# Optimization experiments

Hardware: AMD Instinct MI355X
Metric: run time of the kernel (lower is better)

The kernel has to match this reference:

```python
import jax, jax.numpy as jnp
import numpy as np

N_NODES = 100000
N_EDGES = 3200000
IN_DIM, HID_DIM, OUT_DIM = 512, 32, 16


def spmm(rows, cols, vals, dense):
    # out[r] = sum_{e: rows[e]==r} vals[e] * dense[cols[e]]  == adj @ dense (COO)
    gathered = vals[:, None] * dense[cols]          # [E, D]
    return jax.ops.segment_sum(gathered, rows, num_segments=N_NODES)


def gcn_layer(x, adj_rows, adj_cols, adj_vals, W):
    support = x @ W                                  # dense mm [N, out]
    return spmm(adj_rows, adj_cols, adj_vals, support)


def setup_inputs() -> dict:
    key = jax.random.key(0)
    ks = jax.random.split(key, 8)
    x = jax.random.normal(ks[0], (N_NODES, IN_DIM), dtype=jnp.float32)
    adj_rows = jax.random.randint(ks[1], (N_EDGES,), 0, N_NODES, dtype=jnp.int32)
    adj_cols = jax.random.randint(ks[2], (N_EDGES,), 0, N_NODES, dtype=jnp.int32)
    adj_vals = jax.random.uniform(ks[3], (N_EDGES,), dtype=jnp.float32)
    W1 = jax.random.normal(ks[4], (IN_DIM, HID_DIM), dtype=jnp.float32)
    W2 = jax.random.normal(ks[5], (HID_DIM, OUT_DIM), dtype=jnp.float32)
    W3 = jax.random.normal(ks[6], (OUT_DIM, HID_DIM), dtype=jnp.float32)
    W4 = jax.random.normal(ks[7], (HID_DIM, IN_DIM), dtype=jnp.float32)
    return {"x": x, "adj_rows": adj_rows, "adj_cols": adj_cols,
            "adj_vals": adj_vals, "W1": W1, "W2": W2, "W3": W3, "W4": W4}


def reference(x, adj_rows, adj_cols, adj_vals, W1, W2, W3, W4):
    encoded1 = gcn_layer(x, adj_rows, adj_cols, adj_vals, W1)        # [N, 32]
    encoded2 = gcn_layer(encoded1, adj_rows, adj_cols, adj_vals, W2) # [N, 16]
    decoded1 = gcn_layer(encoded2, adj_rows, adj_cols, adj_vals, W3) # [N, 32]
    decoded2 = gcn_layer(decoded1, adj_rows, adj_cols, adj_vals, W4) # [N, 512]
    return (decoded2, encoded2)
```

## Files before the change

### kernel.cpp

```cpp
#include <hip/hip_runtime.h>
#include <hip/hip_bf16.h>


#define N_NODES 100000
#define N_EDGES 3200000
#define RPB_LOG 7
#define RPB (1 << RPB_LOG)
#define NB ((N_NODES + RPB - 1) / RPB)
#define CHUNK 16384
#define NCHUNK ((N_EDGES + CHUNK - 1) / CHUNK)
#define STAGE_CAP 8192

typedef __attribute__((ext_vector_type(4))) float f32x4;
typedef __attribute__((ext_vector_type(8))) short s16x8;
typedef __attribute__((ext_vector_type(8))) unsigned short u16x8;
typedef __attribute__((ext_vector_type(4))) unsigned short u16x4;
typedef __attribute__((ext_vector_type(4))) int i32x4;

static __device__ inline s16x8 cvt8(const float4& lo, const float4& hi) {
  unsigned p0, p1, p2, p3;
  asm("v_cvt_pk_bf16_f32 %0, %1, %2" : "=v"(p0) : "v"(lo.x), "v"(lo.y));
  asm("v_cvt_pk_bf16_f32 %0, %1, %2" : "=v"(p1) : "v"(lo.z), "v"(lo.w));
  asm("v_cvt_pk_bf16_f32 %0, %1, %2" : "=v"(p2) : "v"(hi.x), "v"(hi.y));
  asm("v_cvt_pk_bf16_f32 %0, %1, %2" : "=v"(p3) : "v"(hi.z), "v"(hi.w));
  i32x4 pi = {(int)p0, (int)p1, (int)p2, (int)p3};
  return __builtin_bit_cast(s16x8, pi);
}

static __device__ inline unsigned pk2(float a, float b) {
  unsigned p;
  asm("v_cvt_pk_bf16_f32 %0, %1, %2" : "=v"(p) : "v"(a), "v"(b));
  return p;
}
static __device__ inline float b2f(unsigned short u) {
  return __uint_as_float(((unsigned)u) << 16);
}

__global__ __launch_bounds__(256) void wconv12_kernel(
    const float* __restrict__ W1, const float* __restrict__ W2,
    uint4* __restrict__ Wfrag) {
  int s = blockIdx.x * 256 + threadIdx.x;
  if (s >= 1024) return;
  int lane = s & 63, kt = s >> 6;
  int n = lane & 15;
  int kb = kt * 32 + (lane >> 4) * 8;
  unsigned p[4];
#pragma unroll
  for (int i = 0; i < 4; ++i) {
    float lo = 0.f, hi = 0.f;
#pragma unroll
    for (int m = 0; m < 32; ++m) {
      float w2 = W2[m * 16 + n];
      lo += W1[(kb + 2 * i) * 32 + m] * w2;
      hi += W1[(kb + 2 * i + 1) * 32 + m] * w2;
    }
    p[i] = pk2(lo, hi);
  }
  Wfrag[s] = make_uint4(p[0], p[1], p[2], p[3]);
}

__global__ __launch_bounds__(256) void mm1_kernel(
    const float* __restrict__ x, const uint4* __restrict__ Wfrag,
    unsigned short* __restrict__ out) {
  const int t = threadIdx.x;
  const int lane = t & 63;
  const int w = t >> 6;
  const int rbase = blockIdx.x * 128 + w * 32;
  const int lrow = lane & 15;
  const int kg = lane >> 4;

  int r0c = rbase + lrow;       if (r0c > N_NODES - 1) r0c = N_NODES - 1;
  int r1c = rbase + 16 + lrow;  if (r1c > N_NODES - 1) r1c = N_NODES - 1;
  const float* xp0 = x + (size_t)r0c * 512 + kg * 8;
  const float* xp1 = x + (size_t)r1c * 512 + kg * 8;
  const s16x8* Wf = (const s16x8*)Wfrag;

  f32x4 acc0 = {0.f, 0.f, 0.f, 0.f}, acc1 = {0.f, 0.f, 0.f, 0.f};

#pragma unroll 4
  for (int kt = 0; kt < 16; ++kt) {
    float4 a0lo = *(const float4*)(xp0 + kt * 32);
    float4 a0hi = *(const float4*)(xp0 + kt * 32 + 4);
    float4 a1lo = *(const float4*)(xp1 + kt * 32);
    float4 a1hi = *(const float4*)(xp1 + kt * 32 + 4);
    s16x8 b = Wf[kt * 64 + lane];
    s16x8 a0 = cvt8(a0lo, a0hi);
    s16x8 a1 = cvt8(a1lo, a1hi);
    acc0 = __builtin_amdgcn_mfma_f32_16x16x32_bf16(a0, b, acc0, 0, 0, 0);
    acc1 = __builtin_amdgcn_mfma_f32_16x16x32_bf16(a1, b, acc1, 0, 0, 0);
  }

  const int col = lane & 15;
#pragma unroll
  for (int reg = 0; reg < 4; ++reg) {
    int r0 = rbase + kg * 4 + reg;
    if (r0 < N_NODES)
      out[(size_t)r0 * 16 + col] = (unsigned short)(pk2(acc0[reg], acc0[reg]) & 0xFFFF);
    int r1 = rbase + 16 + kg * 4 + reg;
    if (r1 < N_NODES)
      out[(size_t)r1 * 16 + col] = (unsigned short)(pk2(acc1[reg], acc1[reg]) & 0xFFFF);
  }
}

__global__ __launch_bounds__(512) void localsort_kernel(
    const int* __restrict__ rows, const int* __restrict__ cols,
    const float* __restrict__ vals, int2* __restrict__ cv_loc,
    int* __restrict__ ofs) {
  __shared__ int lcnt[NB];
  __shared__ int lofs[NB + 1];
  __shared__ int ssum[512];
  const int c = blockIdx.x, t = threadIdx.x;
  const int c0 = c * CHUNK, c1 = min(c0 + CHUNK, N_EDGES);

  for (int i = t; i < NB; i += 512) lcnt[i] = 0;
  __syncthreads();
  for (int e = c0 + t; e < c1; e += 512)
    atomicAdd(&lcnt[rows[e] >> RPB_LOG], 1);
  __syncthreads();

  int v0 = (2 * t < NB) ? lcnt[2 * t] : 0;
  int v1 = (2 * t + 1 < NB) ? lcnt[2 * t + 1] : 0;
  ssum[t] = v0 + v1;
  __syncthreads();
  for (int off = 1; off < 512; off <<= 1) {
    int xv = (t >= off) ? ssum[t - off] : 0;
    __syncthreads();
    ssum[t] += xv;
    __syncthreads();
  }
  int excl = (t == 0) ? 0 : ssum[t - 1];
  if (2 * t < NB) lofs[2 * t] = excl;
  if (2 * t + 1 < NB) lofs[2 * t + 1] = excl + v0;
  if (t == 511) lofs[NB] = ssum[511];
  __syncthreads();

  for (int i = t; i <= NB; i += 512) ofs[c * (NB + 1) + i] = lofs[i];
  for (int i = t; i < NB; i += 512) lcnt[i] = 0;
  __syncthreads();

  for (int e = c0 + t; e < c1; e += 512) {
    int r = rows[e];
    int b = r >> RPB_LOG;
    int rank = atomicAdd(&lcnt[b], 1);
    cv_loc[c0 + lofs[b] + rank] =
        make_int2(((r & (RPB - 1)) << 17) | cols[e], __float_as_int(vals[e]));
  }
}

__global__ __launch_bounds__(1024) void totals_scan_kernel(
    const int* __restrict__ ofs, int* __restrict__ bstart,
    int* __restrict__ row_ptr) {
  __shared__ int s[1024];
  int t = threadIdx.x;
  int tot = 0;
  if (t < NB) {
    for (int cc = 0; cc < NCHUNK; ++cc) {
      const int* o = ofs + cc * (NB + 1);
      tot += o[t + 1] - o[t];
    }
  }
  s[t] = tot;
  __syncthreads();
  for (int off = 1; off < 1024; off <<= 1) {
    int v = (t >= off) ? s[t - off] : 0;
    __syncthreads();
    s[t] += v;
    __syncthreads();
  }
  if (t < NB) bstart[t] = s[t] - tot;
  if (t == 0) { bstart[NB] = N_EDGES; row_ptr[N_NODES] = N_EDGES; }
}

__global__ __launch_bounds__(256) void refine2_kernel(
    const int* __restrict__ ofs, const int* __restrict__ bstart,
    const int2* __restrict__ cv_loc, int2* __restrict__ cv_csr,
    int* __restrict__ row_ptr) {
  __shared__ int gs[NCHUNK];
  __shared__ int q[NCHUNK + 1];
  __shared__ int sq[256];
  __shared__ int rcnt[RPB];
  __shared__ int rbase[RPB];
  __shared__ int2 stage[STAGE_CAP];
  const int b = blockIdx.x, t = threadIdx.x;

  int cnt_t = 0;
  if (t < NCHUNK) {
    int g0 = ofs[t * (NB + 1) + b];
    int g1 = ofs[t * (NB + 1) + b + 1];
    gs[t] = t * CHUNK + g0;
    cnt_t = g1 - g0;
  }
  sq[t] = cnt_t;
  __syncthreads();
  for (int off = 1; off < 256; off <<= 1) {
    int v = (t >= off) ? sq[t - off] : 0;
    __syncthreads();
    sq[t] += v;
    __syncthreads();
  }
  if (t < NCHUNK) q[t] = sq[t] - cnt_t;
  if (t == 0) q[NCHUNK] = sq[255];
  if (t < RPB) rcnt[t] = 0;
  __syncthreads();
  const int Q = q[NCHUNK];

  for (int i = t; i < Q; i += 256) {
    int lo = 0, hi = NCHUNK - 1;
    while (lo < hi) {
      int mid = (lo + hi + 1) >> 1;
      if (q[mid] <= i) lo = mid; else hi = mid - 1;
    }
    int2 e = cv_loc[gs[lo] + (i - q[lo])];
    if (i < STAGE_CAP) stage[i] = e;
    atomicAdd(&rcnt[e.x >> 17], 1);
  }
  __syncthreads();

  int rv = (t < RPB) ? rcnt[t] : 0;
  sq[t] = rv;
  __syncthreads();
  for (int off = 1; off < RPB; off <<= 1) {
    int v = (t >= off) ? sq[t - off] : 0;
    __syncthreads();
    sq[t] += v;
    __syncthreads();
  }
  if (t < RPB) {
    int base = bstart[b] + sq[t] - rv;
    rbase[t] = base;
    int gr = (b << RPB_LOG) + t;
    if (gr < N_NODES) row_ptr[gr] = base;
    rcnt[t] = 0;
  }
  __syncthreads();

  for (int i = t; i < Q; i += 256) {
    int2 e;
    if (i < STAGE_CAP) {
      e = stage[i];
    } else {
      int lo = 0, hi = NCHUNK - 1;
      while (lo < hi) {
        int mid = (lo + hi + 1) >> 1;
        if (q[mid] <= i) lo = mid; else hi = mid - 1;
      }
      e = cv_loc[gs[lo] + (i - q[lo])];
    }
    int rl = e.x >> 17;
    int rank = atomicAdd(&rcnt[rl], 1);
    cv_csr[rbase[rl] + rank] = make_int2(e.x & 0x1FFFF, e.y);
  }
}

template <int OM>
__global__ __launch_bounds__(256) void spmm_b16_kernel(
    const int* __restrict__ rp, const int2* __restrict__ colval,
    const unsigned short* __restrict__ in, unsigned short* __restrict__ outb,
    float* __restrict__ outf) {
  const int t = threadIdx.x;
  const int r = blockIdx.x * 64 + (t >> 2);
  const int q = t & 3;
  if (r >= N_NODES) return;
  const int k0 = rp[r], k1 = rp[r + 1];
  float a0 = 0.f, a1 = 0.f, a2 = 0.f, a3 = 0.f;

  int k = k0;
  for (; k + 7 < k1; k += 8) {
    int2 cv[8];
#pragma unroll
    for (int u = 0; u < 8; ++u) cv[u] = colval[k + u];
    u16x4 g[8];
#pragma unroll
    for (int u = 0; u < 8; ++u)
      g[u] = *(const u16x4*)(in + (size_t)cv[u].x * 16 + q * 4);
#pragma unroll
    for (int u = 0; u < 8; ++u) {
      float v = __int_as_float(cv[u].y);
      a0 += v * b2f(g[u][0]);
      a1 += v * b2f(g[u][1]);
      a2 += v * b2f(g[u][2]);
      a3 += v * b2f(g[u][3]);
    }
  }
  for (; k + 1 < k1; k += 2) {
    int2 cva = colval[k], cvb = colval[k + 1];
    u16x4 ga = *(const u16x4*)(in + (size_t)cva.x * 16 + q * 4);
    u16x4 gb = *(const u16x4*)(in + (size_t)cvb.x * 16 + q * 4);
    float va = __int_as_float(cva.y), vb = __int_as_float(cvb.y);
    a0 += va * b2f(ga[0]); a1 += va * b2f(ga[1]);
    a2 += va * b2f(ga[2]); a3 += va * b2f(ga[3]);
    a0 += vb * b2f(gb[0]); a1 += vb * b2f(gb[1]);
    a2 += vb * b2f(gb[2]); a3 += vb * b2f(gb[3]);
  }
  if (k < k1) {
    int2 cv = colval[k];
    u16x4 g = *(const u16x4*)(in + (size_t)cv.x * 16 + q * 4);
    float v = __int_as_float(cv.y);
    a0 += v * b2f(g[0]); a1 += v * b2f(g[1]);
    a2 += v * b2f(g[2]); a3 += v * b2f(g[3]);
  }

  if (OM == 0 || OM == 1) {
    uint2 pk = make_uint2(pk2(a0, a1), pk2(a2, a3));
    *(uint2*)(outb + (size_t)r * 16 + q * 4) = pk;
  }
  if (OM == 1 || OM == 2) {
    *(float4*)(outf + (size_t)r * 16 + q * 4) = make_float4(a0, a1, a2, a3);
  }
}

__global__ __launch_bounds__(512) void mm4_kernel(
    const float* __restrict__ t3, const float* __restrict__ W3,
    const float* __restrict__ W4, float* __restrict__ out,
    int rows_per_block) {
  const int j = threadIdx.x;
  float w4c[32];
#pragma unroll
  for (int m = 0; m < 32; ++m) w4c[m] = W4[m * 512 + j];
  float w[16];
#pragma unroll
  for (int k = 0; k < 16; ++k) {
    float acc = 0.f;
#pragma unroll
    for (int m = 0; m < 32; ++m) acc += W3[k * 32 + m] * w4c[m];
    w[k] = acc;
  }
  int r0 = blockIdx.x * rows_per_block;
  int r1 = r0 + rows_per_block;
  if (r1 > N_NODES) r1 = N_NODES;
  for (int r = r0; r < r1; ++r) {
    const float* srow = t3 + (size_t)r * 16;
    float a0 = 0.f, a1 = 0.f, a2 = 0.f, a3 = 0.f;
#pragma unroll
    for (int k = 0; k < 16; k += 4) {
      a0 += srow[k + 0] * w[k + 0];
      a1 += srow[k + 1] * w[k + 1];
      a2 += srow[k + 2] * w[k + 2];
      a3 += srow[k + 3] * w[k + 3];
    }
    out[(size_t)r * 512 + j] = (a0 + a1) + (a2 + a3);
  }
}

extern "C" void kernel_launch(void* const* d_in, const int* in_sizes, int n_in,
                              void* d_out, int out_size, void* d_ws, size_t ws_size,
                              hipStream_t stream) {
  const float* x     = (const float*)d_in[0];
  const int*   arows = (const int*)d_in[1];
  const int*   acols = (const int*)d_in[2];
  const float* avals = (const float*)d_in[3];
  const float* W1    = (const float*)d_in[4];
  const float* W2    = (const float*)d_in[5];
  const float* W3    = (const float*)d_in[6];
  const float* W4    = (const float*)d_in[7];

  float* out = (float*)d_out;
  float* dec = out;
  float* enc = out + (size_t)N_NODES * 512;

  unsigned short* bh  = (unsigned short*)d_ws;
  unsigned short* bu  = bh + (size_t)N_NODES * 16;
  unsigned short* be  = bu + (size_t)N_NODES * 16;
  unsigned short* bt2 = be + (size_t)N_NODES * 16;
  float*          t3  = (float*)(bt2 + (size_t)N_NODES * 16);

  int2*  cv_loc  = (int2*)dec;
  int2*  cv_csr  = cv_loc + N_EDGES;
  uint4* Wfrag   = (uint4*)(cv_csr + N_EDGES);
  int*   ofs     = (int*)(Wfrag + 1024);
  int*   row_ptr = ofs + NCHUNK * (NB + 1);
  int*   bstart  = row_ptr + N_NODES + 1;

  wconv12_kernel<<<4, 256, 0, stream>>>(W1, W2, Wfrag);
  localsort_kernel<<<NCHUNK, 512, 0, stream>>>(arows, acols, avals, cv_loc, ofs);
  totals_scan_kernel<<<1, 1024, 0, stream>>>(ofs, bstart, row_ptr);
  refine2_kernel<<<NB, 256, 0, stream>>>(ofs, bstart, cv_loc, cv_csr, row_ptr);

  const int spGrid = (N_NODES + 63) / 64;
  mm1_kernel<<<(N_NODES + 127) / 128, 256, 0, stream>>>(x, Wfrag, bh);
  spmm_b16_kernel<0><<<spGrid, 256, 0, stream>>>(row_ptr, cv_csr, bh, bu, nullptr);
  spmm_b16_kernel<1><<<spGrid, 256, 0, stream>>>(row_ptr, cv_csr, bu, be, enc);
  spmm_b16_kernel<0><<<spGrid, 256, 0, stream>>>(row_ptr, cv_csr, be, bt2, nullptr);
  spmm_b16_kernel<2><<<spGrid, 256, 0, stream>>>(row_ptr, cv_csr, bt2, nullptr, t3);
  mm4_kernel<<<(N_NODES + 63) / 64, 512, 0, stream>>>(t3, W3, W4, dec, 64);
}
```

Before: 409.3 us.

## Pack CSR col/val into 32 bits and simplify the bucket-sort pipeline

New measurement: 408.2 us. About the same (-0.3%).

```diff
diff --git a/kernel.cpp b/kernel.cpp
--- a/kernel.cpp
+++ b/kernel.cpp
@@ -9,11 +9,10 @@
 #define NB ((N_NODES + RPB - 1) / RPB)
 #define CHUNK 16384
 #define NCHUNK ((N_EDGES + CHUNK - 1) / CHUNK)
-#define STAGE_CAP 8192
+#define EPT (CHUNK / 512)
 
 typedef __attribute__((ext_vector_type(4))) float f32x4;
 typedef __attribute__((ext_vector_type(8))) short s16x8;
-typedef __attribute__((ext_vector_type(8))) unsigned short u16x8;
 typedef __attribute__((ext_vector_type(4))) unsigned short u16x4;
 typedef __attribute__((ext_vector_type(4))) int i32x4;
 
@@ -105,7 +104,7 @@
 __global__ __launch_bounds__(512) void localsort_kernel(
     const int* __restrict__ rows, const int* __restrict__ cols,
     const float* __restrict__ vals, int2* __restrict__ cv_loc,
-    int* __restrict__ ofs) {
+    int* __restrict__ ofs, int* __restrict__ gcnt) {
   __shared__ int lcnt[NB];
   __shared__ int lofs[NB + 1];
   __shared__ int ssum[512];
@@ -114,12 +113,20 @@
 
   for (int i = t; i < NB; i += 512) lcnt[i] = 0;
   __syncthreads();
-  for (int e = c0 + t; e < c1; e += 512)
-    atomicAdd(&lcnt[rows[e] >> RPB_LOG], 1);
+
+  int rr[EPT];
+#pragma unroll
+  for (int u = 0; u < EPT; ++u) {
+    int e = c0 + t + u * 512;
+    rr[u] = (e < c1) ? rows[e] : -1;
+    if (rr[u] >= 0) atomicAdd(&lcnt[rr[u] >> RPB_LOG], 1);
+  }
   __syncthreads();
 
   int v0 = (2 * t < NB) ? lcnt[2 * t] : 0;
   int v1 = (2 * t + 1 < NB) ? lcnt[2 * t + 1] : 0;
+  if (v0) atomicAdd(&gcnt[2 * t], v0);
+  if (v1) atomicAdd(&gcnt[2 * t + 1], v1);
   ssum[t] = v0 + v1;
   __syncthreads();
   for (int off = 1; off < 512; off <<= 1) {
@@ -138,49 +145,45 @@
   for (int i = t; i < NB; i += 512) lcnt[i] = 0;
   __syncthreads();
 
-  for (int e = c0 + t; e < c1; e += 512) {
-    int r = rows[e];
-    int b = r >> RPB_LOG;
-    int rank = atomicAdd(&lcnt[b], 1);
-    cv_loc[c0 + lofs[b] + rank] =
-        make_int2(((r & (RPB - 1)) << 17) | cols[e], __float_as_int(vals[e]));
-  }
-}
-
-__global__ __launch_bounds__(1024) void totals_scan_kernel(
-    const int* __restrict__ ofs, int* __restrict__ bstart,
+#pragma unroll
+  for (int u = 0; u < EPT; ++u) {
+    int r = rr[u];
+    if (r >= 0) {
+      int e = c0 + t + u * 512;
+      int b = r >> RPB_LOG;
+      int rank = atomicAdd(&lcnt[b], 1);
+      cv_loc[c0 + lofs[b] + rank] =
+          make_int2(((r & (RPB - 1)) << 17) | cols[e], __float_as_int(vals[e]));
+    }
+  }
+}
+
+__global__ __launch_bounds__(1024) void scan782_kernel(
+    const int* __restrict__ gcnt, int* __restrict__ bstart,
     int* __restrict__ row_ptr) {
   __shared__ int s[1024];
   int t = threadIdx.x;
-  int tot = 0;
-  if (t < NB) {
-    for (int cc = 0; cc < NCHUNK; ++cc) {
-      const int* o = ofs + cc * (NB + 1);
-      tot += o[t + 1] - o[t];
-    }
-  }
-  s[t] = tot;
+  int v = (t < NB) ? gcnt[t] : 0;
+  s[t] = v;
   __syncthreads();
   for (int off = 1; off < 1024; off <<= 1) {
-    int v = (t >= off) ? s[t - off] : 0;
-    __syncthreads();
-    s[t] += v;
-    __syncthreads();
-  }
-  if (t < NB) bstart[t] = s[t] - tot;
+    int xv = (t >= off) ? s[t - off] : 0;
+    __syncthreads();
+    s[t] += xv;
+    __syncthreads();
+  }
+  if (t < NB) bstart[t] = s[t] - v;
   if (t == 0) { bstart[NB] = N_EDGES; row_ptr[N_NODES] = N_EDGES; }
 }
 
-__global__ __launch_bounds__(256) void refine2_kernel(
+__global__ __launch_bounds__(256) void refine3_kernel(
     const int* __restrict__ ofs, const int* __restrict__ bstart,
-    const int2* __restrict__ cv_loc, int2* __restrict__ cv_csr,
+    const int2* __restrict__ cv_loc, unsigned* __restrict__ cv_csr,
     int* __restrict__ row_ptr) {
   __shared__ int gs[NCHUNK];
-  __shared__ int q[NCHUNK + 1];
   __shared__ int sq[256];
   __shared__ int rcnt[RPB];
   __shared__ int rbase[RPB];
-  __shared__ int2 stage[STAGE_CAP];
   const int b = blockIdx.x, t = threadIdx.x;
 
   int cnt_t = 0;
@@ -190,28 +193,11 @@
     gs[t] = t * CHUNK + g0;
     cnt_t = g1 - g0;
   }
-  sq[t] = cnt_t;
-  __syncthreads();
-  for (int off = 1; off < 256; off <<= 1) {
-    int v = (t >= off) ? sq[t - off] : 0;
-    __syncthreads();
-    sq[t] += v;
-    __syncthreads();
-  }
-  if (t < NCHUNK) q[t] = sq[t] - cnt_t;
-  if (t == 0) q[NCHUNK] = sq[255];
   if (t < RPB) rcnt[t] = 0;
   __syncthreads();
-  const int Q = q[NCHUNK];
-
-  for (int i = t; i < Q; i += 256) {
-    int lo = 0, hi = NCHUNK - 1;
-    while (lo < hi) {
-      int mid = (lo + hi + 1) >> 1;
-      if (q[mid] <= i) lo = mid; else hi = mid - 1;
-    }
-    int2 e = cv_loc[gs[lo] + (i - q[lo])];
-    if (i < STAGE_CAP) stage[i] = e;
+
+  for (int i = 0; i < cnt_t; ++i) {
+    int2 e = cv_loc[gs[t] + i];
     atomicAdd(&rcnt[e.x >> 17], 1);
   }
   __syncthreads();
@@ -220,9 +206,9 @@
   sq[t] = rv;
   __syncthreads();
   for (int off = 1; off < RPB; off <<= 1) {
-    int v = (t >= off) ? sq[t - off] : 0;
-    __syncthreads();
-    sq[t] += v;
+    int v = (t >= off && t < RPB) ? sq[t - off] : 0;
+    __syncthreads();
+    if (t < RPB) sq[t] += v;
     __syncthreads();
   }
   if (t < RPB) {
@@ -234,27 +220,20 @@
   }
   __syncthreads();
 
-  for (int i = t; i < Q; i += 256) {
-    int2 e;
-    if (i < STAGE_CAP) {
-      e = stage[i];
-    } else {
-      int lo = 0, hi = NCHUNK - 1;
-      while (lo < hi) {
-        int mid = (lo + hi + 1) >> 1;
-        if (q[mid] <= i) lo = mid; else hi = mid - 1;
-      }
-      e = cv_loc[gs[lo] + (i - q[lo])];
-    }
+  for (int i = 0; i < cnt_t; ++i) {
+    int2 e = cv_loc[gs[t] + i];
     int rl = e.x >> 17;
     int rank = atomicAdd(&rcnt[rl], 1);
-    cv_csr[rbase[rl] + rank] = make_int2(e.x & 0x1FFFF, e.y);
+    float v = __int_as_float(e.y);
+    unsigned vb = pk2(v, v);
+    cv_csr[rbase[rl] + rank] =
+        ((unsigned)(e.x & 0x1FFFF) << 15) | (vb & 0x7FFF);
   }
 }
 
 template <int OM>
 __global__ __launch_bounds__(256) void spmm_b16_kernel(
-    const int* __restrict__ rp, const int2* __restrict__ colval,
+    const int* __restrict__ rp, const unsigned* __restrict__ colval,
     const unsigned short* __restrict__ in, unsigned short* __restrict__ outb,
     float* __restrict__ outf) {
   const int t = threadIdx.x;
@@ -266,16 +245,16 @@
 
   int k = k0;
   for (; k + 7 < k1; k += 8) {
-    int2 cv[8];
+    unsigned cv[8];
 #pragma unroll
     for (int u = 0; u < 8; ++u) cv[u] = colval[k + u];
     u16x4 g[8];
 #pragma unroll
     for (int u = 0; u < 8; ++u)
-      g[u] = *(const u16x4*)(in + (size_t)cv[u].x * 16 + q * 4);
+      g[u] = *(const u16x4*)(in + (size_t)(cv[u] >> 15) * 16 + q * 4);
 #pragma unroll
     for (int u = 0; u < 8; ++u) {
-      float v = __int_as_float(cv[u].y);
+      float v = __uint_as_float((cv[u] & 0x7FFF) << 16);
       a0 += v * b2f(g[u][0]);
       a1 += v * b2f(g[u][1]);
       a2 += v * b2f(g[u][2]);
@@ -283,19 +262,20 @@
     }
   }
   for (; k + 1 < k1; k += 2) {
-    int2 cva = colval[k], cvb = colval[k + 1];
-    u16x4 ga = *(const u16x4*)(in + (size_t)cva.x * 16 + q * 4);
-    u16x4 gb = *(const u16x4*)(in + (size_t)cvb.x * 16 + q * 4);
-    float va = __int_as_float(cva.y), vb = __int_as_float(cvb.y);
+    unsigned ca = colval[k], cb = colval[k + 1];
+    u16x4 ga = *(const u16x4*)(in + (size_t)(ca >> 15) * 16 + q * 4);
+    u16x4 gb = *(const u16x4*)(in + (size_t)(cb >> 15) * 16 + q * 4);
+    float va = __uint_as_float((ca & 0x7FFF) << 16);
+    float vb = __uint_as_float((cb & 0x7FFF) << 16);
     a0 += va * b2f(ga[0]); a1 += va * b2f(ga[1]);
     a2 += va * b2f(ga[2]); a3 += va * b2f(ga[3]);
     a0 += vb * b2f(gb[0]); a1 += vb * b2f(gb[1]);
     a2 += vb * b2f(gb[2]); a3 += vb * b2f(gb[3]);
   }
   if (k < k1) {
-    int2 cv = colval[k];
-    u16x4 g = *(const u16x4*)(in + (size_t)cv.x * 16 + q * 4);
-    float v = __int_as_float(cv.y);
+    unsigned cv = colval[k];
+    u16x4 g = *(const u16x4*)(in + (size_t)(cv >> 15) * 16 + q * 4);
+    float v = __uint_as_float((cv & 0x7FFF) << 16);
     a0 += v * b2f(g[0]); a1 += v * b2f(g[1]);
     a2 += v * b2f(g[2]); a3 += v * b2f(g[3]);
   }
@@ -364,17 +344,19 @@
   unsigned short* bt2 = be + (size_t)N_NODES * 16;
   float*          t3  = (float*)(bt2 + (size_t)N_NODES * 16);
 
-  int2*  cv_loc  = (int2*)dec;
-  int2*  cv_csr  = cv_loc + N_EDGES;
-  uint4* Wfrag   = (uint4*)(cv_csr + N_EDGES);
-  int*   ofs     = (int*)(Wfrag + 1024);
-  int*   row_ptr = ofs + NCHUNK * (NB + 1);
-  int*   bstart  = row_ptr + N_NODES + 1;
-
+  int2*     cv_loc  = (int2*)dec;
+  unsigned* cv_csr  = (unsigned*)(cv_loc + N_EDGES);
+  uint4*    Wfrag   = (uint4*)(cv_csr + N_EDGES);
+  int*      ofs     = (int*)(Wfrag + 1024);
+  int*      row_ptr = ofs + NCHUNK * (NB + 1);
+  int*      bstart  = row_ptr + N_NODES + 1;
+  int*      gcnt    = bstart + NB + 1;
+
+  hipMemsetAsync(gcnt, 0, NB * sizeof(int), stream);
   wconv12_kernel<<<4, 256, 0, stream>>>(W1, W2, Wfrag);
-  localsort_kernel<<<NCHUNK, 512, 0, stream>>>(arows, acols, avals, cv_loc, ofs);
-  totals_scan_kernel<<<1, 1024, 0, stream>>>(ofs, bstart, row_ptr);
-  refine2_kernel<<<NB, 256, 0, stream>>>(ofs, bstart, cv_loc, cv_csr, row_ptr);
+  localsort_kernel<<<NCHUNK, 512, 0, stream>>>(arows, acols, avals, cv_loc, ofs, gcnt);
+  scan782_kernel<<<1, 1024, 0, stream>>>(gcnt, bstart, row_ptr);
+  refine3_kernel<<<NB, 256, 0, stream>>>(ofs, bstart, cv_loc, cv_csr, row_ptr);
 
   const int spGrid = (N_NODES + 63) / 64;
   mm1_kernel<<<(N_NODES + 127) / 128, 256, 0, stream>>>(x, Wfrag, bh);
```
